# Performance work log

Measured on AMD Instinct MI355X. Metric: run time of the kernel, lower is better.

Reference implementation:

```python
import jax, jax.numpy as jnp
import numpy as np

N_NODES = 100000
N_EDGES = 1600000
NUM_FEATURES = 128
NHID = 64
HIDDEN = 2 * NHID  # GATConv out_channels = nhid*2 = 128
NUM_CLASSES = 2
NUM_GRAPHS = 64
NEG_SLOPE = 0.2  # PyG GATConv default


def setup_inputs() -> dict:
    key = jax.random.key(0)
    ks = jax.random.split(key, 16)
    x = jax.random.normal(ks[0], (N_NODES, NUM_FEATURES), dtype=jnp.float32)
    edge_index = jax.random.randint(ks[1], (2, N_EDGES), 0, N_NODES, dtype=jnp.int64)
    batch = jnp.sort(jax.random.randint(ks[2], (N_NODES,), 0, NUM_GRAPHS, dtype=jnp.int64))
    def glorot(k, shape):
        lim = np.sqrt(6.0 / (shape[0] + shape[1]))
        return jax.random.uniform(k, shape, jnp.float32, -lim, lim)
    W1 = glorot(ks[3], (NUM_FEATURES, HIDDEN))
    a_src1 = glorot(ks[4], (HIDDEN, 1))[:, 0]
    a_dst1 = glorot(ks[5], (HIDDEN, 1))[:, 0]
    b1 = jnp.zeros((HIDDEN,), jnp.float32)
    W2 = glorot(ks[6], (HIDDEN, HIDDEN))
    a_src2 = glorot(ks[7], (HIDDEN, 1))[:, 0]
    a_dst2 = glorot(ks[8], (HIDDEN, 1))[:, 0]
    b2 = jnp.zeros((HIDDEN,), jnp.float32)
    fc1_w = glorot(ks[9], (HIDDEN, NHID))
    fc1_b = jnp.zeros((NHID,), jnp.float32)
    fc2_w = glorot(ks[10], (NHID, NUM_CLASSES))
    fc2_b = jnp.zeros((NUM_CLASSES,), jnp.float32)
    return {"x": x, "edge_index": edge_index, "batch": batch,
            "W1": W1, "a_src1": a_src1, "a_dst1": a_dst1, "b1": b1,
            "W2": W2, "a_src2": a_src2, "a_dst2": a_dst2, "b2": b2,
            "fc1_w": fc1_w, "fc1_b": fc1_b, "fc2_w": fc2_w, "fc2_b": fc2_b}


def gat_conv(x, src, dst, W, a_src, a_dst, b, n_nodes):
    # PyG GATConv, heads=1, add_self_loops=True: message flows src -> dst
    h = x @ W                                   # [N, H]
    alpha_s = h @ a_src                         # [N]
    alpha_d = h @ a_dst                         # [N]
    e = jax.nn.leaky_relu(alpha_s[src] + alpha_d[dst], NEG_SLOPE)  # [E2]
    m = jax.ops.segment_max(e, dst, num_segments=n_nodes)          # per-dst max
    ex = jnp.exp(e - m[dst])
    z = jax.ops.segment_sum(ex, dst, num_segments=n_nodes)
    alpha = ex / z[dst]                         # segment softmax over incoming edges
    out = jax.ops.segment_sum(h[src] * alpha[:, None], dst, num_segments=n_nodes)
    return out + b


def reference(x, edge_index, batch, W1, a_src1, a_dst1, b1,
              W2, a_src2, a_dst2, b2, fc1_w, fc1_b, fc2_w, fc2_b):
    n = x.shape[0]
    loop = jnp.arange(n, dtype=edge_index.dtype)
    src = jnp.concatenate([edge_index[0], loop])  # add self-loops (PyG default)
    dst = jnp.concatenate([edge_index[1], loop])
    h = jax.nn.selu(gat_conv(x, src, dst, W1, a_src1, a_dst1, b1, n))
    h = jax.nn.selu(gat_conv(h, src, dst, W2, a_src2, a_dst2, b2, n))
    # global mean pool over graphs
    sums = jax.ops.segment_sum(h, batch, num_segments=NUM_GRAPHS)
    cnt = jax.ops.segment_sum(jnp.ones((n,), h.dtype), batch, num_segments=NUM_GRAPHS)
    pooled = jax.nn.selu(sums / jnp.maximum(cnt, 1.0)[:, None])
    feat = jax.nn.selu(pooled @ fc1_w + fc1_b)   # dropout is identity in eval
    logits = feat @ fc2_w + fc2_b
    return logits, feat
```

## Files before the change

kernel.cpp:

```cpp
#include <hip/hip_runtime.h>
#include <hip/hip_bf16.h>

#define N_NODES 100000
#define N_EDGES 1600000
#define E_TOT   (N_EDGES + N_NODES)
#define F 128
#define NGRAPH 64
#define NEG_SLOPE 0.2f
#define SELU_SCALE 1.0507009873554805f
#define SELU_ALPHA 1.6732632423543772f

#define BSZ 256
#define NB  391
#define CAP 5120
#define CHUNK 4096
#define NCHUNK 416
#define LCAP 5120
#define PCHUNK 32

typedef __attribute__((ext_vector_type(8))) short bf16x8;
typedef __attribute__((ext_vector_type(4))) float f32x4;

__device__ __forceinline__ float selu_f(float x) {
    return x > 0.f ? SELU_SCALE * x : SELU_SCALE * SELU_ALPHA * (expf(x) - 1.f);
}
__device__ __forceinline__ float lrelu(float x) {
    return x > 0.f ? x : NEG_SLOPE * x;
}
__device__ __forceinline__ unsigned short f2bf(float f) {
    unsigned u = __float_as_uint(f);
    return (unsigned short)((u + 0x7FFFu + ((u >> 16) & 1u)) >> 16);
}
__device__ __forceinline__ float bfval(unsigned short u) {
    return __uint_as_float(((unsigned)u) << 16);
}
__device__ __forceinline__ float ub0(unsigned w) { return (float)(w & 0xffu); }
__device__ __forceinline__ float ub1(unsigned w) { return (float)((w >> 8) & 0xffu); }
__device__ __forceinline__ float ub2(unsigned w) { return (float)((w >> 16) & 0xffu); }
__device__ __forceinline__ float ub3(unsigned w) { return (float)(w >> 24); }

__global__ __launch_bounds__(256) void init_k(int* __restrict__ cursor,
                                              float* __restrict__ gsum) {
    int i = blockIdx.x * 256 + threadIdx.x;
    if (i < NB) cursor[i] = i * CAP;
    if (i < NGRAPH * F) gsum[i] = 0.f;
}

__global__ __launch_bounds__(256) void pack_w2(const float* __restrict__ W1,
                                               const float* __restrict__ W2,
                                               unsigned short* __restrict__ W1f,
                                               unsigned short* __restrict__ W2f) {
    int i = blockIdx.x * 256 + threadIdx.x;
    const float* W = (i < 2048) ? W1 : W2;
    unsigned short* Wf = (i < 2048) ? W1f : W2f;
    int ii = i & 2047;
    int l = ii & 63, t = (ii >> 6) & 3, nt = ii >> 8;
    int kb = t * 32 + (l >> 4) * 8;
    int n  = nt * 16 + (l & 15);
    unsigned short o[8];
#pragma unroll
    for (int j = 0; j < 8; ++j) o[j] = f2bf(W[(size_t)(kb + j) * F + n]);
    uint4 p;
    p.x = ((unsigned)o[1] << 16) | o[0];
    p.y = ((unsigned)o[3] << 16) | o[2];
    p.z = ((unsigned)o[5] << 16) | o[4];
    p.w = ((unsigned)o[7] << 16) | o[6];
    ((uint4*)Wf)[ii] = p;
}

template <bool XF32>
__global__ __launch_bounds__(256) void gemm_mfma(const void* __restrict__ Xin,
                                                 const unsigned short* __restrict__ Wf,
                                                 const float* __restrict__ avs,
                                                 const float* __restrict__ avd,
                                                 unsigned char* __restrict__ Hq,
                                                 float2* __restrict__ asc,
                                                 float* __restrict__ ad_) {
    int w = threadIdx.x >> 6, l = threadIdx.x & 63;
    int row0 = blockIdx.x * 64 + w * 16;
    int arow = row0 + (l & 15);
    int arow_c = arow < N_NODES ? arow : N_NODES - 1;
    f32x4 acc[8] = {};
#pragma unroll
    for (int t = 0; t < 4; ++t) {
        bf16x8 a;
        if (XF32) {
            const float* Xf = (const float*)Xin + (size_t)arow_c * F + t * 32 + (l >> 4) * 8;
            float4 v0 = *(const float4*)Xf;
            float4 v1 = *(const float4*)(Xf + 4);
            a[0] = (short)f2bf(v0.x); a[1] = (short)f2bf(v0.y);
            a[2] = (short)f2bf(v0.z); a[3] = (short)f2bf(v0.w);
            a[4] = (short)f2bf(v1.x); a[5] = (short)f2bf(v1.y);
            a[6] = (short)f2bf(v1.z); a[7] = (short)f2bf(v1.w);
        } else {
            a = *(const bf16x8*)((const unsigned short*)Xin +
                                 (size_t)arow_c * F + t * 32 + (l >> 4) * 8);
        }
#pragma unroll
        for (int nt = 0; nt < 8; ++nt) {
            bf16x8 b = *(const bf16x8*)(Wf + (size_t)((nt * 4 + t) * 64 + l) * 8);
            acc[nt] = __builtin_amdgcn_mfma_f32_16x16x32_bf16(a, b, acc[nt], 0, 0, 0);
        }
    }
    int c = l & 15;
    float ps[4] = {}, pd[4] = {}, mx[4] = {};
#pragma unroll
    for (int nt = 0; nt < 8; ++nt) {
        float ws = avs[nt * 16 + c];
        float wd = avd[nt * 16 + c];
#pragma unroll
        for (int r = 0; r < 4; ++r) {
            ps[r] += acc[nt][r] * ws;
            pd[r] += acc[nt][r] * wd;
            mx[r] = fmaxf(mx[r], fabsf(acc[nt][r]));
        }
    }
#pragma unroll
    for (int r = 0; r < 4; ++r) {
#pragma unroll
        for (int off = 1; off < 16; off <<= 1) {
            ps[r] += __shfl_xor(ps[r], off);
            pd[r] += __shfl_xor(pd[r], off);
            mx[r] = fmaxf(mx[r], __shfl_xor(mx[r], off));
        }
    }
#pragma unroll
    for (int r = 0; r < 4; ++r) {
        int grow = row0 + (l >> 4) * 4 + r;
        if (grow >= N_NODES) continue;
        float inv = mx[r] > 0.f ? 127.f / mx[r] : 0.f;
#pragma unroll
        for (int nt = 0; nt < 8; ++nt) {
            int q = (int)rintf(acc[nt][r] * inv) + 128;
            Hq[(size_t)grow * F + nt * 16 + c] = (unsigned char)q;
        }
        if (c == 0) {
            asc[grow] = make_float2(ps[r], mx[r] * (1.f / 127.f));
            ad_[grow] = pd[r];
        }
    }
}

__global__ __launch_bounds__(256) void scatter1(const int* __restrict__ ei,
                                                int* __restrict__ cursor,
                                                unsigned* __restrict__ packed) {
    __shared__ int lh[NB], lbase[NB];
    for (int i = threadIdx.x; i < NB; i += 256) lh[i] = 0;
    __syncthreads();
    int base = blockIdx.x * CHUNK;
#pragma unroll
    for (int k = 0; k < 16; ++k) {
        int i = base + k * 256 + threadIdx.x;
        if (i < E_TOT) {
            int d = (i < N_EDGES) ? ei[N_EDGES + i] : i - N_EDGES;
            atomicAdd(&lh[d >> 8], 1);
        }
    }
    __syncthreads();
    for (int i = threadIdx.x; i < NB; i += 256) {
        int cn = lh[i];
        lbase[i] = cn ? atomicAdd(&cursor[i], cn) : 0;
        lh[i] = 0;
    }
    __syncthreads();
#pragma unroll
    for (int k = 0; k < 16; ++k) {
        int i = base + k * 256 + threadIdx.x;
        if (i < E_TOT) {
            int s, d;
            if (i < N_EDGES) { s = ei[i]; d = ei[N_EDGES + i]; }
            else             { s = d = i - N_EDGES; }
            int b = d >> 8;
            int r = atomicAdd(&lh[b], 1);
            int pos = lbase[b] + r;
            if (pos < (b + 1) * CAP)
                packed[pos] = (unsigned)s | ((unsigned)(d & 255) << 20);
        }
    }
}

__global__ __launch_bounds__(256) void build2(const int* __restrict__ cursor,
                                              const unsigned* __restrict__ packed,
                                              int* __restrict__ rs,
                                              int* __restrict__ rd,
                                              int* __restrict__ csr_src) {
    __shared__ int sh_hist[BSZ], sh_row[BSZ], ts[BSZ];
    __shared__ int lsrc[LCAP];
    int b = blockIdx.x, t = threadIdx.x;
    int node0 = b << 8;
    int nn = min(BSZ, N_NODES - node0);
    int base = b * CAP;
    int cnt = min(cursor[b] - base, CAP);
    sh_hist[t] = 0;
    __syncthreads();
    for (int j = t; j < cnt; j += 256)
        atomicAdd(&sh_hist[packed[base + j] >> 20], 1);
    __syncthreads();
    int dv = sh_hist[t];
    ts[t] = dv;
    __syncthreads();
    for (int off = 1; off < 256; off <<= 1) {
        int u = (t >= off) ? ts[t - off] : 0;
        __syncthreads();
        ts[t] += u;
        __syncthreads();
    }
    sh_row[t] = ts[t] - dv;
    if (t < nn) { rs[node0 + t] = base + sh_row[t]; rd[node0 + t] = dv; }
    sh_hist[t] = 0;
    __syncthreads();
    for (int j = t; j < cnt; j += 256) {
        unsigned u = packed[base + j];
        int dlo = u >> 20;
        int r = atomicAdd(&sh_hist[dlo], 1);
        lsrc[sh_row[dlo] + r] = (int)(u & 0xFFFFFu);
    }
    __syncthreads();
    for (int j = t; j < cnt; j += 256) csr_src[base + j] = lsrc[j];
}

__global__ __launch_bounds__(256) void gat_csr(const int* __restrict__ rs,
                                               const int* __restrict__ rd,
                                               const int* __restrict__ csr_src,
                                               const float2* __restrict__ asc,
                                               const float* __restrict__ ad_,
                                               const unsigned char* __restrict__ Hq,
                                               const float* __restrict__ bias,
                                               unsigned short* __restrict__ outb) {
    int v = (blockIdx.x * 256 + threadIdx.x) >> 6;
    int lane = threadIdx.x & 63;
    if (v >= N_NODES) return;
    int start = rs[v];
    int deg = rd[v];
    float ad_v = ad_[v];
    const int half = lane >> 5;
    const int fq = lane & 31;
    const unsigned* HqI = (const unsigned*)Hq;
    float acc0 = 0.f, acc1 = 0.f, acc2 = 0.f, acc3 = 0.f, ksum = 0.f;

    if (deg <= 64) {
        int s_reg = 0;
        float2 a2 = make_float2(0.f, 0.f);
        float ev = -__builtin_inff();
        if (lane < deg) {
            s_reg = csr_src[start + lane];
            a2 = asc[s_reg];
            ev = lrelu(a2.x + ad_v);
        }
        float m = ev;
#pragma unroll
        for (int off = 1; off < 64; off <<= 1) m = fmaxf(m, __shfl_xor(m, off));
        float ex = (lane < deg) ? expf(ev - m) : 0.f;
        float zs = ex;
#pragma unroll
        for (int off = 1; off < 64; off <<= 1) zs += __shfl_xor(zs, off);
        float alsc_l = (ex / zs) * a2.y;
        int e = 0;
        for (; e + 16 <= deg; e += 16) {
            float al[8]; int sv[8]; unsigned uw[8];
#pragma unroll
            for (int q = 0; q < 8; ++q) {
                al[q] = __shfl(alsc_l, e + 2 * q + half);
                sv[q] = __shfl(s_reg,  e + 2 * q + half);
            }
#pragma unroll
            for (int q = 0; q < 8; ++q) uw[q] = HqI[(sv[q] << 5) + fq];
#pragma unroll
            for (int q = 0; q < 8; ++q) {
                ksum += al[q];
                acc0 += ub0(uw[q]) * al[q];
                acc1 += ub1(uw[q]) * al[q];
                acc2 += ub2(uw[q]) * al[q];
                acc3 += ub3(uw[q]) * al[q];
            }
        }
        for (; e + 8 <= deg; e += 8) {
            float al[4]; int sv[4]; unsigned uw[4];
#pragma unroll
            for (int q = 0; q < 4; ++q) {
                al[q] = __shfl(alsc_l, e + 2 * q + half);
                sv[q] = __shfl(s_reg,  e + 2 * q + half);
            }
#pragma unroll
            for (int q = 0; q < 4; ++q) uw[q] = HqI[(sv[q] << 5) + fq];
#pragma unroll
            for (int q = 0; q < 4; ++q) {
                ksum += al[q];
                acc0 += ub0(uw[q]) * al[q];
                acc1 += ub1(uw[q]) * al[q];
                acc2 += ub2(uw[q]) * al[q];
                acc3 += ub3(uw[q]) * al[q];
            }
        }
        for (; e + 2 <= deg; e += 2) {
            float al = __shfl(alsc_l, e + half);
            int   s  = __shfl(s_reg,  e + half);
            unsigned uw = HqI[(s << 5) + fq];
            ksum += al;
            acc0 += ub0(uw) * al; acc1 += ub1(uw) * al;
            acc2 += ub2(uw) * al; acc3 += ub3(uw) * al;
        }
        if (e < deg) {
            float al = __shfl(alsc_l, e);
            int   s  = __shfl(s_reg,  e);
            if (half == 0) {
                unsigned uw = HqI[(s << 5) + fq];
                ksum += al;
                acc0 += ub0(uw) * al; acc1 += ub1(uw) * al;
                acc2 += ub2(uw) * al; acc3 += ub3(uw) * al;
            }
        }
    } else {
        float m = -__builtin_inff();
        for (int i = start + lane; i < start + deg; i += 64)
            m = fmaxf(m, lrelu(asc[csr_src[i]].x + ad_v));
#pragma unroll
        for (int off = 1; off < 64; off <<= 1) m = fmaxf(m, __shfl_xor(m, off));
        float zs = 0.f;
        for (int i = start + lane; i < start + deg; i += 64)
            zs += expf(lrelu(asc[csr_src[i]].x + ad_v) - m);
#pragma unroll
        for (int off = 1; off < 64; off <<= 1) zs += __shfl_xor(zs, off);
        float zinv = 1.f / zs;
        int e = 0;
        for (; e + 2 <= deg; e += 2) {
            int s = csr_src[start + e + half];
            float2 a2 = asc[s];
            float al = expf(lrelu(a2.x + ad_v) - m) * zinv * a2.y;
            unsigned uw = HqI[(s << 5) + fq];
            ksum += al;
            acc0 += ub0(uw) * al; acc1 += ub1(uw) * al;
            acc2 += ub2(uw) * al; acc3 += ub3(uw) * al;
        }
        if (e < deg && half == 0) {
            int s = csr_src[start + e];
            float2 a2 = asc[s];
            float al = expf(lrelu(a2.x + ad_v) - m) * zinv * a2.y;
            unsigned uw = HqI[(s << 5) + fq];
            ksum += al;
            acc0 += ub0(uw) * al; acc1 += ub1(uw) * al;
            acc2 += ub2(uw) * al; acc3 += ub3(uw) * al;
        }
    }
    acc0 += __shfl_xor(acc0, 32); acc1 += __shfl_xor(acc1, 32);
    acc2 += __shfl_xor(acc2, 32); acc3 += __shfl_xor(acc3, 32);
    ksum += __shfl_xor(ksum, 32);
    float4 bv = *(const float4*)(bias + fq * 4);
    float r0 = selu_f(acc0 - 128.f * ksum + bv.x);
    float r1 = selu_f(acc1 - 128.f * ksum + bv.y);
    float r2 = selu_f(acc2 - 128.f * ksum + bv.z);
    float r3 = selu_f(acc3 - 128.f * ksum + bv.w);
    if (half == 0) {
        uint2 p;
        p.x = ((unsigned)f2bf(r1) << 16) | f2bf(r0);
        p.y = ((unsigned)f2bf(r3) << 16) | f2bf(r2);
        *(uint2*)(outb + (size_t)v * F + fq * 4) = p;
    }
}

__device__ __forceinline__ int lower_bound(const int* __restrict__ b, int v) {
    int lo = 0, hi = N_NODES;
    while (lo < hi) { int mid = (lo + hi) >> 1; if (b[mid] < v) lo = mid + 1; else hi = mid; }
    return lo;
}

__global__ __launch_bounds__(128) void pool_partial(const unsigned short* __restrict__ Xb,
                                                    const int* __restrict__ batch,
                                                    float* __restrict__ gsum) {
    int g = blockIdx.x / PCHUNK, c = blockIdx.x % PCHUNK;
    int start = lower_bound(batch, g);
    int end = lower_bound(batch, g + 1);
    int len = end - start;
    int s0 = start + (int)((long)len * c / PCHUNK);
    int s1 = start + (int)((long)len * (c + 1) / PCHUNK);
    if (s1 <= s0) return;
    int f = threadIdx.x;
    float sum = 0.f;
    for (int i = s0; i < s1; ++i)
        sum += bfval(Xb[(size_t)i * F + f]);
    atomicAdd(&gsum[g * F + f], sum);
}

__global__ __launch_bounds__(128) void pool_head(const float* __restrict__ gsum,
                                                 const int* __restrict__ batch,
                                                 const float* __restrict__ fc1w,
                                                 const float* __restrict__ fc1b,
                                                 const float* __restrict__ fc2w,
                                                 const float* __restrict__ fc2b,
                                                 float* __restrict__ out) {
    __shared__ float pooled[128];
    __shared__ float fs[64];
    __shared__ int bnd[2];
    int g = blockIdx.x, t = threadIdx.x;
    if (t < 2) bnd[t] = lower_bound(batch, g + t);
    __syncthreads();
    float c = fmaxf((float)(bnd[1] - bnd[0]), 1.f);
    pooled[t] = selu_f(gsum[g * F + t] / c);
    __syncthreads();
    if (t < 64) {
        float a = fc1b[t];
        for (int k = 0; k < F; ++k) a += pooled[k] * fc1w[k * 64 + t];
        float fv = selu_f(a);
        fs[t] = fv;
        out[128 + g * 64 + t] = fv;
    }
    __syncthreads();
    if (t < 2) {
        float l = fc2b[t];
        for (int k = 0; k < 64; ++k) l += fs[k] * fc2w[k * 2 + t];
        out[g * 2 + t] = l;
    }
}

extern "C" void kernel_launch(void* const* d_in, const int* in_sizes, int n_in,
                              void* d_out, int out_size, void* d_ws, size_t ws_size,
                              hipStream_t stream) {
    const float* x    = (const float*)d_in[0];
    const int*   ei   = (const int*)d_in[1];
    const int*   batch= (const int*)d_in[2];
    const float* W1   = (const float*)d_in[3];
    const float* as1  = (const float*)d_in[4];
    const float* ad1  = (const float*)d_in[5];
    const float* b1   = (const float*)d_in[6];
    const float* W2   = (const float*)d_in[7];
    const float* as2  = (const float*)d_in[8];
    const float* ad2  = (const float*)d_in[9];
    const float* b2   = (const float*)d_in[10];
    const float* fc1w = (const float*)d_in[11];
    const float* fc1b = (const float*)d_in[12];
    const float* fc2w = (const float*)d_in[13];
    const float* fc2b = (const float*)d_in[14];
    float* out = (float*)d_out;

    unsigned short* Xb   = (unsigned short*)d_ws;
    unsigned char*  Hq   = (unsigned char*)(Xb + (size_t)N_NODES * F);
    unsigned short* W1f  = (unsigned short*)(Hq + (size_t)N_NODES * F);
    unsigned short* W2f  = W1f + 16384;
    float2* asc   = (float2*)(W2f + 16384);
    float*  ad_   = (float*)(asc + N_NODES);
    int*    rs    = (int*)(ad_ + N_NODES);
    int*    rd    = rs + N_NODES;
    int*    csr_src = rd + N_NODES;
    unsigned* packed = (unsigned*)(csr_src + NB * CAP);
    int*    cursor= (int*)(packed + NB * CAP);
    float*  gsum  = (float*)(cursor + NB + 64);

    const int gGemm = (N_NODES + 63) / 64;
    const int gNode = (N_NODES + 3) / 4;

    init_k<<<32, 256, 0, stream>>>(cursor, gsum);
    pack_w2<<<16, 256, 0, stream>>>(W1, W2, W1f, W2f);

    scatter1<<<NCHUNK, 256, 0, stream>>>(ei, cursor, packed);
    build2<<<NB, 256, 0, stream>>>(cursor, packed, rs, rd, csr_src);

    gemm_mfma<true><<<gGemm, 256, 0, stream>>>(x, W1f, as1, ad1, Hq, asc, ad_);
    gat_csr<<<gNode, 256, 0, stream>>>(rs, rd, csr_src, asc, ad_, Hq, b1, Xb);

    gemm_mfma<false><<<gGemm, 256, 0, stream>>>(Xb, W2f, as2, ad2, Hq, asc, ad_);
    gat_csr<<<gNode, 256, 0, stream>>>(rs, rd, csr_src, asc, ad_, Hq, b2, Xb);

    pool_partial<<<NGRAPH * PCHUNK, 128, 0, stream>>>(Xb, batch, gsum);
    pool_head<<<NGRAPH, 128, 0, stream>>>(gsum, batch, fc1w, fc1b, fc2w, fc2b, out);
}
```

Before: 241.2 us.

## Process two destination nodes per wavefront in GAT aggregation, pack row start/degree

The GAT aggregation kernel now assigns two destination nodes per 64-lane wavefront, one per 32-lane half, when both degrees are at most 32. Each half runs its own softmax over up to 32 edges and gathers neighbour rows independently, removing the cross-half reduction and the idle lanes of the old one-node-per-wave scheme. Row start and degree are packed into a single int2 array, and expf is swapped for __expf. Wavefronts where either node has a higher degree fall back to processing the two nodes one after another. Lanes sharing a wave but with different degrees loop to the larger degree, which adds some divergence.

```diff
diff --git a/kernel.cpp b/kernel.cpp
--- a/kernel.cpp
+++ b/kernel.cpp
@@ -22,7 +22,7 @@
 typedef __attribute__((ext_vector_type(4))) float f32x4;
 
 __device__ __forceinline__ float selu_f(float x) {
-    return x > 0.f ? SELU_SCALE * x : SELU_SCALE * SELU_ALPHA * (expf(x) - 1.f);
+    return x > 0.f ? SELU_SCALE * x : SELU_SCALE * SELU_ALPHA * (__expf(x) - 1.f);
 }
 __device__ __forceinline__ float lrelu(float x) {
     return x > 0.f ? x : NEG_SLOPE * x;
@@ -181,8 +181,7 @@
 
 __global__ __launch_bounds__(256) void build2(const int* __restrict__ cursor,
                                               const unsigned* __restrict__ packed,
-                                              int* __restrict__ rs,
-                                              int* __restrict__ rd,
+                                              int2* __restrict__ rsd,
                                               int* __restrict__ csr_src) {
     __shared__ int sh_hist[BSZ], sh_row[BSZ], ts[BSZ];
     __shared__ int lsrc[LCAP];
@@ -206,7 +205,7 @@
         __syncthreads();
     }
     sh_row[t] = ts[t] - dv;
-    if (t < nn) { rs[node0 + t] = base + sh_row[t]; rd[node0 + t] = dv; }
+    if (t < nn) rsd[node0 + t] = make_int2(base + sh_row[t], dv);
     sh_hist[t] = 0;
     __syncthreads();
     for (int j = t; j < cnt; j += 256) {
@@ -219,52 +218,55 @@
     for (int j = t; j < cnt; j += 256) csr_src[base + j] = lsrc[j];
 }
 
-__global__ __launch_bounds__(256) void gat_csr(const int* __restrict__ rs,
-                                               const int* __restrict__ rd,
-                                               const int* __restrict__ csr_src,
-                                               const float2* __restrict__ asc,
-                                               const float* __restrict__ ad_,
-                                               const unsigned char* __restrict__ Hq,
-                                               const float* __restrict__ bias,
-                                               unsigned short* __restrict__ outb) {
-    int v = (blockIdx.x * 256 + threadIdx.x) >> 6;
+__global__ __launch_bounds__(256) void gat2(const int2* __restrict__ rsd,
+                                            const int* __restrict__ csr_src,
+                                            const float2* __restrict__ asc,
+                                            const float* __restrict__ ad_,
+                                            const unsigned char* __restrict__ Hq,
+                                            const float* __restrict__ bias,
+                                            unsigned short* __restrict__ outb) {
+    int wid = (blockIdx.x * 256 + threadIdx.x) >> 6;
     int lane = threadIdx.x & 63;
-    if (v >= N_NODES) return;
-    int start = rs[v];
-    int deg = rd[v];
-    float ad_v = ad_[v];
-    const int half = lane >> 5;
-    const int fq = lane & 31;
+    int vbase = wid * 2;
+    if (vbase >= N_NODES) return;
+    const int hb = lane & 32;
+    const int j  = lane & 31;
     const unsigned* HqI = (const unsigned*)Hq;
-    float acc0 = 0.f, acc1 = 0.f, acc2 = 0.f, acc3 = 0.f, ksum = 0.f;
-
-    if (deg <= 64) {
+    int vown = vbase + (lane >> 5);
+
+    int2 rv = rsd[vown];
+    int start = rv.x, deg = rv.y;
+    int dmax = max(deg, __shfl_xor(deg, 32));
+
+    if (dmax <= 32) {
         int s_reg = 0;
         float2 a2 = make_float2(0.f, 0.f);
         float ev = -__builtin_inff();
-        if (lane < deg) {
-            s_reg = csr_src[start + lane];
+        if (j < deg) {
+            s_reg = csr_src[start + j];
             a2 = asc[s_reg];
-            ev = lrelu(a2.x + ad_v);
+            ev = lrelu(a2.x + ad_[vown]);
         }
         float m = ev;
 #pragma unroll
-        for (int off = 1; off < 64; off <<= 1) m = fmaxf(m, __shfl_xor(m, off));
-        float ex = (lane < deg) ? expf(ev - m) : 0.f;
+        for (int off = 1; off < 32; off <<= 1) m = fmaxf(m, __shfl_xor(m, off));
+        float ex = (j < deg) ? __expf(ev - m) : 0.f;
         float zs = ex;
 #pragma unroll
-        for (int off = 1; off < 64; off <<= 1) zs += __shfl_xor(zs, off);
-        float alsc_l = (ex / zs) * a2.y;
+        for (int off = 1; off < 32; off <<= 1) zs += __shfl_xor(zs, off);
+        float alsc = (ex / zs) * a2.y;
+
+        float acc0 = 0.f, acc1 = 0.f, acc2 = 0.f, acc3 = 0.f, ksum = 0.f;
         int e = 0;
-        for (; e + 16 <= deg; e += 16) {
+        for (; e + 8 <= dmax; e += 8) {
             float al[8]; int sv[8]; unsigned uw[8];
 #pragma unroll
             for (int q = 0; q < 8; ++q) {
-                al[q] = __shfl(alsc_l, e + 2 * q + half);
-                sv[q] = __shfl(s_reg,  e + 2 * q + half);
+                al[q] = __shfl(alsc, hb | (e + q));
+                sv[q] = __shfl(s_reg, hb | (e + q));
             }
 #pragma unroll
-            for (int q = 0; q < 8; ++q) uw[q] = HqI[(sv[q] << 5) + fq];
+            for (int q = 0; q < 8; ++q) uw[q] = HqI[(sv[q] << 5) + j];
 #pragma unroll
             for (int q = 0; q < 8; ++q) {
                 ksum += al[q];
@@ -274,87 +276,77 @@
                 acc3 += ub3(uw[q]) * al[q];
             }
         }
-        for (; e + 8 <= deg; e += 8) {
-            float al[4]; int sv[4]; unsigned uw[4];
-#pragma unroll
-            for (int q = 0; q < 4; ++q) {
-                al[q] = __shfl(alsc_l, e + 2 * q + half);
-                sv[q] = __shfl(s_reg,  e + 2 * q + half);
-            }
-#pragma unroll
-            for (int q = 0; q < 4; ++q) uw[q] = HqI[(sv[q] << 5) + fq];
-#pragma unroll
-            for (int q = 0; q < 4; ++q) {
-                ksum += al[q];
-                acc0 += ub0(uw[q]) * al[q];
-                acc1 += ub1(uw[q]) * al[q];
-                acc2 += ub2(uw[q]) * al[q];
-                acc3 += ub3(uw[q]) * al[q];
-            }
-        }
-        for (; e + 2 <= deg; e += 2) {
-            float al = __shfl(alsc_l, e + half);
-            int   s  = __shfl(s_reg,  e + half);
-            unsigned uw = HqI[(s << 5) + fq];
+        for (; e < dmax; ++e) {
+            float al = __shfl(alsc, hb | e);
+            int   s  = __shfl(s_reg, hb | e);
+            unsigned uw = HqI[(s << 5) + j];
             ksum += al;
             acc0 += ub0(uw) * al; acc1 += ub1(uw) * al;
             acc2 += ub2(uw) * al; acc3 += ub3(uw) * al;
         }
-        if (e < deg) {
-            float al = __shfl(alsc_l, e);
-            int   s  = __shfl(s_reg,  e);
-            if (half == 0) {
+        float4 bv = *(const float4*)(bias + j * 4);
+        float r0 = selu_f(acc0 - 128.f * ksum + bv.x);
+        float r1 = selu_f(acc1 - 128.f * ksum + bv.y);
+        float r2 = selu_f(acc2 - 128.f * ksum + bv.z);
+        float r3 = selu_f(acc3 - 128.f * ksum + bv.w);
+        uint2 p;
+        p.x = ((unsigned)f2bf(r1) << 16) | f2bf(r0);
+        p.y = ((unsigned)f2bf(r3) << 16) | f2bf(r2);
+        *(uint2*)(outb + (size_t)vown * F + j * 4) = p;
+    } else {
+        const int half = lane >> 5;
+        const int fq = lane & 31;
+        for (int sub = 0; sub < 2; ++sub) {
+            int vv = vbase + sub;
+            int2 r2v = rsd[vv];
+            int st = r2v.x, dg = r2v.y;
+            float adv = ad_[vv];
+            float m = -__builtin_inff();
+            for (int i = st + lane; i < st + dg; i += 64)
+                m = fmaxf(m, lrelu(asc[csr_src[i]].x + adv));
+#pragma unroll
+            for (int off = 1; off < 64; off <<= 1) m = fmaxf(m, __shfl_xor(m, off));
+            float zs = 0.f;
+            for (int i = st + lane; i < st + dg; i += 64)
+                zs += __expf(lrelu(asc[csr_src[i]].x + adv) - m);
+#pragma unroll
+            for (int off = 1; off < 64; off <<= 1) zs += __shfl_xor(zs, off);
+            float zinv = 1.f / zs;
+            float acc0 = 0.f, acc1 = 0.f, acc2 = 0.f, acc3 = 0.f, ksum = 0.f;
+            int e = 0;
+            for (; e + 2 <= dg; e += 2) {
+                int s = csr_src[st + e + half];
+                float2 a2 = asc[s];
+                float al = __expf(lrelu(a2.x + adv) - m) * zinv * a2.y;
                 unsigned uw = HqI[(s << 5) + fq];
                 ksum += al;
                 acc0 += ub0(uw) * al; acc1 += ub1(uw) * al;
                 acc2 += ub2(uw) * al; acc3 += ub3(uw) * al;
             }
-        }
-    } else {
-        float m = -__builtin_inff();
-        for (int i = start + lane; i < start + deg; i += 64)
-            m = fmaxf(m, lrelu(asc[csr_src[i]].x + ad_v));
-#pragma unroll
-        for (int off = 1; off < 64; off <<= 1) m = fmaxf(m, __shfl_xor(m, off));
-        float zs = 0.f;
-        for (int i = start + lane; i < start + deg; i += 64)
-            zs += expf(lrelu(asc[csr_src[i]].x + ad_v) - m);
-#pragma unroll
-        for (int off = 1; off < 64; off <<= 1) zs += __shfl_xor(zs, off);
-        float zinv = 1.f / zs;
-        int e = 0;
-        for (; e + 2 <= deg; e += 2) {
-            int s = csr_src[start + e + half];
-            float2 a2 = asc[s];
-            float al = expf(lrelu(a2.x + ad_v) - m) * zinv * a2.y;
-            unsigned uw = HqI[(s << 5) + fq];
-            ksum += al;
-            acc0 += ub0(uw) * al; acc1 += ub1(uw) * al;
-            acc2 += ub2(uw) * al; acc3 += ub3(uw) * al;
-        }
-        if (e < deg && half == 0) {
-            int s = csr_src[start + e];
-            float2 a2 = asc[s];
-            float al = expf(lrelu(a2.x + ad_v) - m) * zinv * a2.y;
-            unsigned uw = HqI[(s << 5) + fq];
-            ksum += al;
-            acc0 += ub0(uw) * al; acc1 += ub1(uw) * al;
-            acc2 += ub2(uw) * al; acc3 += ub3(uw) * al;
-        }
-    }
-    acc0 += __shfl_xor(acc0, 32); acc1 += __shfl_xor(acc1, 32);
-    acc2 += __shfl_xor(acc2, 32); acc3 += __shfl_xor(acc3, 32);
-    ksum += __shfl_xor(ksum, 32);
-    float4 bv = *(const float4*)(bias + fq * 4);
-    float r0 = selu_f(acc0 - 128.f * ksum + bv.x);
-    float r1 = selu_f(acc1 - 128.f * ksum + bv.y);
-    float r2 = selu_f(acc2 - 128.f * ksum + bv.z);
-    float r3 = selu_f(acc3 - 128.f * ksum + bv.w);
-    if (half == 0) {
-        uint2 p;
-        p.x = ((unsigned)f2bf(r1) << 16) | f2bf(r0);
-        p.y = ((unsigned)f2bf(r3) << 16) | f2bf(r2);
-        *(uint2*)(outb + (size_t)v * F + fq * 4) = p;
+            if (e < dg && half == 0) {
+                int s = csr_src[st + e];
+                float2 a2 = asc[s];
+                float al = __expf(lrelu(a2.x + adv) - m) * zinv * a2.y;
+                unsigned uw = HqI[(s << 5) + fq];
+                ksum += al;
+                acc0 += ub0(uw) * al; acc1 += ub1(uw) * al;
+                acc2 += ub2(uw) * al; acc3 += ub3(uw) * al;
+            }
+            acc0 += __shfl_xor(acc0, 32); acc1 += __shfl_xor(acc1, 32);
+            acc2 += __shfl_xor(acc2, 32); acc3 += __shfl_xor(acc3, 32);
+            ksum += __shfl_xor(ksum, 32);
+            float4 bv = *(const float4*)(bias + fq * 4);
+            float r0 = selu_f(acc0 - 128.f * ksum + bv.x);
+            float r1 = selu_f(acc1 - 128.f * ksum + bv.y);
+            float r2 = selu_f(acc2 - 128.f * ksum + bv.z);
+            float r3 = selu_f(acc3 - 128.f * ksum + bv.w);
+            if (half == 0) {
+                uint2 p;
+                p.x = ((unsigned)f2bf(r1) << 16) | f2bf(r0);
+                p.y = ((unsigned)f2bf(r3) << 16) | f2bf(r2);
+                *(uint2*)(outb + (size_t)vv * F + fq * 4) = p;
+            }
+        }
     }
 }
 
@@ -438,27 +430,26 @@
     unsigned short* W2f  = W1f + 16384;
     float2* asc   = (float2*)(W2f + 16384);
     float*  ad_   = (float*)(asc + N_NODES);
-    int*    rs    = (int*)(ad_ + N_NODES);
-    int*    rd    = rs + N_NODES;
-    int*    csr_src = rd + N_NODES;
+    int2*   rsd   = (int2*)(ad_ + N_NODES);
+    int*    csr_src = (int*)(rsd + N_NODES);
     unsigned* packed = (unsigned*)(csr_src + NB * CAP);
     int*    cursor= (int*)(packed + NB * CAP);
     float*  gsum  = (float*)(cursor + NB + 64);
 
     const int gGemm = (N_NODES + 63) / 64;
-    const int gNode = (N_NODES + 3) / 4;
+    const int gGat  = (N_NODES + 7) / 8;
 
     init_k<<<32, 256, 0, stream>>>(cursor, gsum);
     pack_w2<<<16, 256, 0, stream>>>(W1, W2, W1f, W2f);
 
     scatter1<<<NCHUNK, 256, 0, stream>>>(ei, cursor, packed);
-    build2<<<NB, 256, 0, stream>>>(cursor, packed, rs, rd, csr_src);
+    build2<<<NB, 256, 0, stream>>>(cursor, packed, rsd, csr_src);
 
     gemm_mfma<true><<<gGemm, 256, 0, stream>>>(x, W1f, as1, ad1, Hq, asc, ad_);
-    gat_csr<<<gNode, 256, 0, stream>>>(rs, rd, csr_src, asc, ad_, Hq, b1, Xb);
+    gat2<<<gGat, 256, 0, stream>>>(rsd, csr_src, asc, ad_, Hq, b1, Xb);
 
     gemm_mfma<false><<<gGemm, 256, 0, stream>>>(Xb, W2f, as2, ad2, Hq, asc, ad_);
-    gat_csr<<<gNode, 256, 0, stream>>>(rs, rd, csr_src, asc, ad_, Hq, b2, Xb);
+    gat2<<<gGat, 256, 0, stream>>>(rsd, csr_src, asc, ad_, Hq, b2, Xb);
 
     pool_partial<<<NGRAPH * PCHUNK, 128, 0, stream>>>(Xb, batch, gsum);
     pool_head<<<NGRAPH, 128, 0, stream>>>(gsum, batch, fc1w, fc1b, fc2w, fc2b, out);
```

New measurement: 217.8 us. 1.11x faster.
